# Kernel optimization log

Measured on AMD Instinct MI355X. Metric: run time of the kernel, lower is better.

The kernel has to match this reference:

```python
import jax, jax.numpy as jnp
import numpy as np

N, E, IN, HID, HEADS, OUT, G = 50000, 800000, 128, 32, 4, 128, 64
NEG_SLOPE = 0.2


def setup_inputs() -> dict:
    key = jax.random.key(0)
    ks = jax.random.split(key, 20)
    p = lambda k, shape: jax.random.normal(k, shape, jnp.float32) * 0.1
    inp = {
        "x": jax.random.normal(ks[0], (N, IN), jnp.float32),
        "edge_index": jax.random.randint(ks[1], (2, E), 0, N, dtype=jnp.int64),
        "batch": jnp.sort(jax.random.randint(ks[2], (N,), 0, G, dtype=jnp.int64)),
        # input_proj: Linear(in_dim, hidden*heads)
        "Wp": p(ks[3], (IN, HID * HEADS)), "bp": p(ks[4], (HID * HEADS,)),
        # layer 1: GATConv(128 -> 32, heads=4, concat) -> 128
        "W1": p(ks[5], (IN, HEADS * HID)), "a_src1": p(ks[6], (HEADS, HID)),
        "a_dst1": p(ks[7], (HEADS, HID)), "b1": p(ks[8], (HEADS * HID,)),
        # layer 2: GATConv(128 -> 32, heads=4, concat) -> 128
        "W2": p(ks[9], (HEADS * HID, HEADS * HID)), "a_src2": p(ks[10], (HEADS, HID)),
        "a_dst2": p(ks[11], (HEADS, HID)), "b2": p(ks[12], (HEADS * HID,)),
        # layer 3: GATConv(128 -> 128, heads=1, concat=False mean)
        "W3": p(ks[13], (HEADS * HID, OUT)), "a_src3": p(ks[14], (1, OUT)),
        "a_dst3": p(ks[15], (1, OUT)), "b3": p(ks[16], (OUT,)),
    }
    return inp


def _gat_conv(x, src, dst, W, a_src, a_dst, b, heads, concat):
    n = x.shape[0]
    h = (x @ W).reshape(n, heads, -1)                      # [N,H,C]
    al_s = jnp.einsum("nhc,hc->nh", h, a_src)              # [N,H]
    al_d = jnp.einsum("nhc,hc->nh", h, a_dst)
    e = al_s[src] + al_d[dst]                              # [Etot,H]
    e = jax.nn.leaky_relu(e, NEG_SLOPE)
    # softmax over incoming edges of each destination node
    m = jax.ops.segment_max(e, dst, num_segments=n)
    e = jnp.exp(e - m[dst])
    s = jax.ops.segment_sum(e, dst, num_segments=n)
    alpha = e / s[dst]                                     # [Etot,H]
    msg = h[src] * alpha[:, :, None]                       # [Etot,H,C]
    out = jax.ops.segment_sum(msg, dst, num_segments=n)    # [N,H,C]
    out = out.reshape(n, -1) if concat else out.mean(axis=1)
    return out + b


def reference(x, edge_index, batch, Wp, bp, W1, a_src1, a_dst1, b1,
              W2, a_src2, a_dst2, b2, W3, a_src3, a_dst3, b3):
    n = x.shape[0]
    loops = jnp.arange(n, dtype=edge_index.dtype)
    src = jnp.concatenate([edge_index[0], loops])          # add self-loops (PyG default)
    dst = jnp.concatenate([edge_index[1], loops])
    x_skip = x @ Wp + bp
    h = _gat_conv(x, src, dst, W1, a_src1, a_dst1, b1, HEADS, True)
    h = jax.nn.relu(h + x_skip)
    h = _gat_conv(h, src, dst, W2, a_src2, a_dst2, b2, HEADS, True)
    h = jax.nn.relu(h + x_skip)
    h = _gat_conv(h, src, dst, W3, a_src3, a_dst3, b3, 1, False)
    # global_mean_pool
    sums = jax.ops.segment_sum(h, batch, num_segments=G)
    cnt = jax.ops.segment_sum(jnp.ones((n,), h.dtype), batch, num_segments=G)
    ctx = sums / jnp.maximum(cnt, 1.0)[:, None]
    return h, ctx
```

## Files before the change

### kernel.cpp

```cpp
#include <hip/hip_runtime.h>
#include <hip/hip_bf16.h>
#include <math.h>

#define N_NODES 50000
#define N_EDGES 800000
#define G_GROUPS 64
#define NEG_SLOPE 0.2f
#define BUCKET 64

typedef __attribute__((ext_vector_type(8))) short bf16x8;
typedef __attribute__((ext_vector_type(4))) float f32x4;

static __device__ __forceinline__ float bf16_lo(unsigned int u) {
    return __uint_as_float(u << 16);
}
static __device__ __forceinline__ float bf16_hi(unsigned int u) {
    return __uint_as_float(u & 0xffff0000u);
}
static __device__ __forceinline__ unsigned short f_to_bf16(float f) {
    unsigned int u = __float_as_uint(f);
    unsigned int r = (u + 0x7fffu + ((u >> 16) & 1u)) >> 16;
    return (unsigned short)r;
}

#define GB_BLOCKS 782
#define CV_BLOCKS 3125
#define FB_BLOCKS 3125


__global__ __launch_bounds__(256) void conv_init(const float* __restrict__ x,
                                                 unsigned short* __restrict__ xb,
                                                 const float* __restrict__ W0,
                                                 const float* __restrict__ W1,
                                                 const float* __restrict__ W2,
                                                 const float* __restrict__ W3,
                                                 unsigned short* __restrict__ T0,
                                                 unsigned short* __restrict__ T1,
                                                 unsigned short* __restrict__ T2,
                                                 unsigned short* __restrict__ T3,
                                                 int* __restrict__ cnt,
                                                 float* __restrict__ ctx) {
    int tid = blockIdx.x * 256 + threadIdx.x;
    if (tid < 65536) {
        int m = tid >> 14;
        int idx = tid & 16383;
        int k = idx >> 7, c = idx & 127;
        const float* W = (m == 0) ? W0 : (m == 1) ? W1 : (m == 2) ? W2 : W3;
        unsigned short* T = (m == 0) ? T0 : (m == 1) ? T1 : (m == 2) ? T2 : T3;
        T[c * 128 + k] = f_to_bf16(W[idx]);
    }
    if (tid < N_NODES) cnt[tid] = 0;
    if (tid < G_GROUPS * 128) ctx[tid] = 0.f;
    const float4* p = (const float4*)(x + (size_t)tid * 8);
    float4 v0 = p[0], v1 = p[1];
    ushort4 o0, o1;
    o0.x = f_to_bf16(v0.x); o0.y = f_to_bf16(v0.y);
    o0.z = f_to_bf16(v0.z); o0.w = f_to_bf16(v0.w);
    o1.x = f_to_bf16(v1.x); o1.y = f_to_bf16(v1.y);
    o1.z = f_to_bf16(v1.z); o1.w = f_to_bf16(v1.w);
    ushort4* q = (ushort4*)(xb + (size_t)tid * 8);
    q[0] = o0; q[1] = o1;
}


static __device__ __forceinline__ void gemm_body(const unsigned short* __restrict__ Xb,
                                                 const unsigned short* __restrict__ Wt,
                                                 const float* __restrict__ bias,
                                                 unsigned short* __restrict__ Yb,
                                                 int n, int addBias,
                                                 const float* __restrict__ asrcP,
                                                 const float* __restrict__ adstP,
                                                 float* __restrict__ alsP,
                                                 float* __restrict__ aldP, int H,
                                                 int blk, unsigned short* Wl) {
    char* wl = (char*)Wl;
    int t = threadIdx.x;
#pragma unroll
    for (int i = 0; i < 8; i++) {
        int slot = i * 256 + t;
        int byte = slot * 16;
        int r = byte >> 8;
        int off = byte & 255;
        uint4 v = *(const uint4*)((const char*)Wt + byte);
        *(uint4*)(wl + r * 256 + (off ^ ((r & 7) << 4))) = v;
    }
    __syncthreads();

    int wave = t >> 6, lane = t & 63;
    int lr = lane & 15, lk = lane >> 4;
    int arow = blk * 64 + wave * 16 + lr;
    int arowc = min(arow, n - 1);
    const char* xrow = (const char*)(Xb + (size_t)arowc * 128);
    bf16x8 a[4];
#pragma unroll
    for (int ks = 0; ks < 4; ks++)
        a[ks] = *(const bf16x8*)(xrow + ks * 64 + lk * 16);

    f32x4 zero = {0.f, 0.f, 0.f, 0.f};
    f32x4 acc[8];
#pragma unroll
    for (int j = 0; j < 8; j++) acc[j] = zero;

#pragma unroll
    for (int j = 0; j < 8; j++) {
        int c = j * 16 + lr;
        const char* wrow = wl + c * 256;
        int sw = (c & 7) << 4;
#pragma unroll
        for (int ks = 0; ks < 4; ks++) {
            bf16x8 b = *(const bf16x8*)(wrow + ((ks * 64 + lk * 16) ^ sw));
            acc[j] = __builtin_amdgcn_mfma_f32_16x16x32_bf16(a[ks], b, acc[j], 0, 0, 0);
        }
    }

    int orow0 = blk * 64 + wave * 16 + lk * 4;
    if (!alsP) {
#pragma unroll
        for (int j = 0; j < 8; j++) {
            int c = j * 16 + lr;
            float bv = addBias ? bias[c] : 0.f;
#pragma unroll
            for (int r = 0; r < 4; r++) {
                int orow = orow0 + r;
                if (orow < n) Yb[(size_t)orow * 128 + c] = f_to_bf16(acc[j][r] + bv);
            }
        }
        return;
    }

    __syncthreads();
    unsigned short* Hl = Wl;
    int lrow0 = wave * 16 + lk * 4;
#pragma unroll
    for (int j = 0; j < 8; j++) {
        int c = j * 16 + lr;
#pragma unroll
        for (int r = 0; r < 4; r++) {
            int orow = orow0 + r;
            unsigned short hv = f_to_bf16(acc[j][r]);
            Hl[(lrow0 + r) * 128 + c] = hv;
            if (orow < n) Yb[(size_t)orow * 128 + c] = hv;
        }
    }
    __syncthreads();

    int row = t >> 2, q = t & 3;
    int node = blk * 64 + row;
    if (node < n) {
        const unsigned int* hp = (const unsigned int*)(Hl + row * 128 + q * 32);
        const float* ap = asrcP + q * 32;
        const float* dp = adstP + q * 32;
        float s = 0.f, dd = 0.f;
#pragma unroll 4
        for (int i = 0; i < 16; i++) {
            unsigned int u = hp[i];
            float v0 = bf16_lo(u), v1 = bf16_hi(u);
            s  = fmaf(v0, ap[2 * i], s);
            s  = fmaf(v1, ap[2 * i + 1], s);
            dd = fmaf(v0, dp[2 * i], dd);
            dd = fmaf(v1, dp[2 * i + 1], dd);
        }
        if (H == 4) {
            alsP[node * 4 + q] = s;
            aldP[node * 4 + q] = dd;
        } else {
            s += __shfl_xor(s, 1); s += __shfl_xor(s, 2);
            dd += __shfl_xor(dd, 1); dd += __shfl_xor(dd, 2);
            if (q == 0) { alsP[node] = s; aldP[node] = dd; }
        }
    }
}


__global__ __launch_bounds__(256) void prep2(const unsigned short* __restrict__ Xb,
                                             const unsigned short* __restrict__ WtA,
                                             const unsigned short* __restrict__ WtB,
                                             const float* __restrict__ biasA,
                                             unsigned short* __restrict__ xskip,
                                             unsigned short* __restrict__ hfeat,
                                             const float* __restrict__ as1,
                                             const float* __restrict__ ad1,
                                             float* __restrict__ als,
                                             float* __restrict__ ald,
                                             const int* __restrict__ ei,
                                             int* __restrict__ cnt,
                                             int* __restrict__ colb) {
    __shared__ unsigned short Wl[128 * 128];
    int bid = blockIdx.x;
    if (bid % 3 == 0) {
        int g = bid / 3;
        if (g >= 2 * GB_BLOCKS) return;
        if (g < GB_BLOCKS) {
            gemm_body(Xb, WtA, biasA, xskip, N_NODES, 1,
                      nullptr, nullptr, nullptr, nullptr, 0, g, Wl);
        } else {
            gemm_body(Xb, WtB, nullptr, hfeat, N_NODES, 0,
                      as1, ad1, als, ald, 4, g - GB_BLOCKS, Wl);
        }
    } else {
        int fb = bid - bid / 3 - 1;
        int e = fb * 256 + threadIdx.x;
        if (fb >= FB_BLOCKS || e >= N_EDGES) return;
        int src = ei[e];
        int dst = ei[N_EDGES + e];
        int pos = atomicAdd(&cnt[dst], 1);
        if (pos < BUCKET) colb[dst * BUCKET + pos] = src;
    }
}


__global__ __launch_bounds__(256) void gemm_mfma(const unsigned short* __restrict__ Xb,
                                                 const unsigned short* __restrict__ Wt,
                                                 unsigned short* __restrict__ Yb,
                                                 const float* __restrict__ asrcP,
                                                 const float* __restrict__ adstP,
                                                 float* __restrict__ alsP,
                                                 float* __restrict__ aldP, int H) {
    __shared__ unsigned short Wl[128 * 128];
    gemm_body(Xb, Wt, nullptr, Yb, N_NODES, 0,
              asrcP, adstP, alsP, aldP, H, blockIdx.x, Wl);
}


template <int H, int MODE>
__global__ __launch_bounds__(256) void aggregate(const unsigned short* __restrict__ hfeat,
                                                 const float* __restrict__ als,
                                                 const float* __restrict__ ald,
                                                 const int* __restrict__ cnt,
                                                 const int* __restrict__ colb,
                                                 const float* __restrict__ bias,
                                                 const unsigned short* __restrict__ xskip,
                                                 float* __restrict__ outf,
                                                 unsigned short* __restrict__ outb, int n) {
    int wave = (blockIdx.x * blockDim.x + threadIdx.x) >> 6;
    int lane = threadIdx.x & 63;
    if (wave >= n) return;
    int d = wave;
    int h2 = (H == 4) ? (lane >> 4) : 0;
    int eoff = lane & 15;
    int sbase = (H == 4) ? (lane & 48) : 0;
    float aldh = ald[d * H + h2];
    int c0 = 2 * lane;
    int cd = min(cnt[d], BUCKET);
    const int* bkt = colb + d * BUCKET;

    float vs = als[d * H + h2] + aldh;
    vs = (vs > 0.f) ? vs : NEG_SLOPE * vs;
    float ps = __expf(fminf(vs, 60.f));
    unsigned int us = *(const unsigned int*)&hfeat[(size_t)d * 128 + c0];
    float psum = (eoff == 0) ? ps : 0.f;
    float a0 = ps * bf16_lo(us);
    float a1 = ps * bf16_hi(us);

    for (int ce = 0; ce < cd; ce += 16) {
        int idx = ce + eoff;
        int idxc = min(idx, cd - 1);
        int sE = bkt[idxc];
        float v = als[sE * H + h2] + aldh;
        v = (v > 0.f) ? v : NEG_SLOPE * v;
        float p = (idx < cd) ? __expf(fminf(v, 60.f)) : 0.f;
        psum += p;
        int nv = min(cd - ce, 16);
        if (nv == 16) {
#pragma unroll
            for (int e = 0; e < 16; e++) {
                int s = __shfl(sE, sbase + e);
                float pe = __shfl(p, sbase + e);
                unsigned int u = *(const unsigned int*)&hfeat[(size_t)s * 128 + c0];
                a0 = fmaf(pe, bf16_lo(u), a0);
                a1 = fmaf(pe, bf16_hi(u), a1);
            }
        } else {
            for (int e = 0; e < nv; e++) {
                int s = __shfl(sE, sbase + e);
                float pe = __shfl(p, sbase + e);
                unsigned int u = *(const unsigned int*)&hfeat[(size_t)s * 128 + c0];
                a0 = fmaf(pe, bf16_lo(u), a0);
                a1 = fmaf(pe, bf16_hi(u), a1);
            }
        }
    }

#pragma unroll
    for (int o = 1; o < 16; o <<= 1)
        psum += __shfl_xor(psum, o);

    float inv = 1.f / psum;
    float o0 = a0 * inv + bias[c0];
    float o1 = a1 * inv + bias[c0 + 1];
    if (MODE == 0) {
        unsigned int ux = *(const unsigned int*)&xskip[(size_t)d * 128 + c0];
        o0 = fmaxf(o0 + bf16_lo(ux), 0.f);
        o1 = fmaxf(o1 + bf16_hi(ux), 0.f);
        unsigned int packed = (unsigned int)f_to_bf16(o0) |
                              ((unsigned int)f_to_bf16(o1) << 16);
        *(unsigned int*)&outb[(size_t)d * 128 + c0] = packed;
    } else {
        outf[(size_t)d * 128 + c0] = o0;
        outf[(size_t)d * 128 + c0 + 1] = o1;
    }
}


__global__ void pool_partial(const float* __restrict__ h, const int* __restrict__ batch,
                             float* __restrict__ ctx) {
    int c = threadIdx.x;
    int base = blockIdx.x * 64;
    int lim = min(base + 64, N_NODES);
    if (base >= N_NODES) return;
    float acc = 0.f;
    int curg = batch[base];
    for (int node = base; node < lim; node++) {
        int g = batch[node];
        if (g != curg) {
            atomicAdd(&ctx[curg * 128 + c], acc);
            curg = g; acc = 0.f;
        }
        acc += h[(size_t)node * 128 + c];
    }
    atomicAdd(&ctx[curg * 128 + c], acc);
}

__global__ void pool_div(const int* __restrict__ batch, float* __restrict__ ctx) {
    int g = blockIdx.x;
    int c = threadIdx.x;
    int lo = 0, hi = N_NODES;
    while (lo < hi) { int mid = (lo + hi) >> 1; if (batch[mid] < g) lo = mid + 1; else hi = mid; }
    int gs = lo;
    hi = N_NODES;
    while (lo < hi) { int mid = (lo + hi) >> 1; if (batch[mid] < g + 1) lo = mid + 1; else hi = mid; }
    int ge = lo;
    ctx[g * 128 + c] /= fmaxf((float)(ge - gs), 1.f);
}


extern "C" void kernel_launch(void* const* d_in, const int* in_sizes, int n_in,
                              void* d_out, int out_size, void* d_ws, size_t ws_size,
                              hipStream_t stream) {
    const float* x   = (const float*)d_in[0];
    const int*   ei  = (const int*)d_in[1];
    const int*   bat = (const int*)d_in[2];
    const float* Wp  = (const float*)d_in[3];
    const float* bp  = (const float*)d_in[4];
    const float* W1  = (const float*)d_in[5];
    const float* as1 = (const float*)d_in[6];
    const float* ad1 = (const float*)d_in[7];
    const float* b1  = (const float*)d_in[8];
    const float* W2  = (const float*)d_in[9];
    const float* as2 = (const float*)d_in[10];
    const float* ad2 = (const float*)d_in[11];
    const float* b2  = (const float*)d_in[12];
    const float* W3  = (const float*)d_in[13];
    const float* as3 = (const float*)d_in[14];
    const float* ad3 = (const float*)d_in[15];
    const float* b3  = (const float*)d_in[16];

    float* out_h   = (float*)d_out;
    float* out_ctx = out_h + (size_t)N_NODES * 128;

    char* w = (char*)d_ws;
    unsigned short* xskip = (unsigned short*)w;  w += (size_t)N_NODES * 128 * 2;
    unsigned short* hfeat = (unsigned short*)w;  w += (size_t)N_NODES * 128 * 2;
    unsigned short* hcur  = (unsigned short*)w;  w += (size_t)N_NODES * 128 * 2;
    unsigned short* xb    = (unsigned short*)w;  w += (size_t)N_NODES * 128 * 2;
    unsigned short* Wtp   = (unsigned short*)w;  w += 16384 * 2;
    unsigned short* Wt1   = (unsigned short*)w;  w += 16384 * 2;
    unsigned short* Wt2   = (unsigned short*)w;  w += 16384 * 2;
    unsigned short* Wt3   = (unsigned short*)w;  w += 16384 * 2;
    float* als   = (float*)w;                    w += (size_t)N_NODES * 4 * 4;
    float* ald   = (float*)w;                    w += (size_t)N_NODES * 4 * 4;
    int* cnt     = (int*)w;                      w += (size_t)N_NODES * 4;
    int* colb    = (int*)w;                      w += (size_t)N_NODES * BUCKET * 4;

    conv_init<<<CV_BLOCKS, 256, 0, stream>>>(x, xb, Wp, W1, W2, W3,
                                             Wtp, Wt1, Wt2, Wt3, cnt, out_ctx);

    prep2<<<4692, 256, 0, stream>>>(xb, Wtp, Wt1, bp, xskip, hfeat,
                                    as1, ad1, als, ald, ei, cnt, colb);

    const int AGB = (N_NODES * 64 + 255) / 256;

    aggregate<4, 0><<<AGB, 256, 0, stream>>>(hfeat, als, ald, cnt, colb, b1, xskip,
                                             nullptr, hcur, N_NODES);

    gemm_mfma<<<GB_BLOCKS, 256, 0, stream>>>(hcur, Wt2, hfeat, as2, ad2, als, ald, 4);
    aggregate<4, 0><<<AGB, 256, 0, stream>>>(hfeat, als, ald, cnt, colb, b2, xskip,
                                             nullptr, hcur, N_NODES);

    gemm_mfma<<<GB_BLOCKS, 256, 0, stream>>>(hcur, Wt3, hfeat, as3, ad3, als, ald, 1);
    aggregate<1, 1><<<AGB, 256, 0, stream>>>(hfeat, als, ald, cnt, colb, b3, nullptr,
                                             out_h, nullptr, N_NODES);

    pool_partial<<<GB_BLOCKS, 128, 0, stream>>>(out_h, bat, out_ctx);
    pool_div<<<G_GROUPS, 128, 0, stream>>>(bat, out_ctx);
}
```

Baseline: 255.0 us.

## Prefetch next edge chunk in aggregate, widen H=1 chunks, shrink pool blocks

The aggregate loop now loads the next chunk's source indices and attention logits while the current chunk's feature gathers run, a software pipeline meant to hide index and logit load latency. For the single-head layer each chunk spans all 64 lanes instead of 16, so one wave covers up to 64 edges per chunk and the psum reduction spans the full wave. pool_partial uses 32 nodes per block, which doubles the block count for more parallelism at the cost of more atomics.

```diff
diff --git a/kernel.cpp b/kernel.cpp
--- a/kernel.cpp
+++ b/kernel.cpp
@@ -236,8 +236,9 @@
     int lane = threadIdx.x & 63;
     if (wave >= n) return;
     int d = wave;
+    const int CH = (H == 4) ? 16 : 64;
     int h2 = (H == 4) ? (lane >> 4) : 0;
-    int eoff = lane & 15;
+    int eoff = (H == 4) ? (lane & 15) : lane;
     int sbase = (H == 4) ? (lane & 48) : 0;
     float aldh = ald[d * H + h2];
     int c0 = 2 * lane;
@@ -252,18 +253,25 @@
     float a0 = ps * bf16_lo(us);
     float a1 = ps * bf16_hi(us);
 
-    for (int ce = 0; ce < cd; ce += 16) {
-        int idx = ce + eoff;
-        int idxc = min(idx, cd - 1);
-        int sE = bkt[idxc];
+    int sE = 0;
+    float p = 0.f;
+    if (cd > 0) {
+        int idx = eoff;
+        sE = bkt[min(idx, cd - 1)];
         float v = als[sE * H + h2] + aldh;
         v = (v > 0.f) ? v : NEG_SLOPE * v;
-        float p = (idx < cd) ? __expf(fminf(v, 60.f)) : 0.f;
+        p = (idx < cd) ? __expf(fminf(v, 60.f)) : 0.f;
+    }
+
+    for (int ce = 0; ce < cd; ce += CH) {
         psum += p;
-        int nv = min(cd - ce, 16);
-        if (nv == 16) {
-#pragma unroll
-            for (int e = 0; e < 16; e++) {
+        int nce = ce + CH;
+        int sE_n = 0;
+        if (nce < cd) sE_n = bkt[min(nce + eoff, cd - 1)];
+        int nv = min(cd - ce, CH);
+        if (nv == CH) {
+#pragma unroll
+            for (int e = 0; e < CH; e++) {
                 int s = __shfl(sE, sbase + e);
                 float pe = __shfl(p, sbase + e);
                 unsigned int u = *(const unsigned int*)&hfeat[(size_t)s * 128 + c0];
@@ -279,10 +287,18 @@
                 a1 = fmaf(pe, bf16_hi(u), a1);
             }
         }
-    }
-
-#pragma unroll
-    for (int o = 1; o < 16; o <<= 1)
+        float p_n = 0.f;
+        if (nce < cd) {
+            float v = als[sE_n * H + h2] + aldh;
+            v = (v > 0.f) ? v : NEG_SLOPE * v;
+            p_n = (nce + eoff < cd) ? __expf(fminf(v, 60.f)) : 0.f;
+        }
+        sE = sE_n;
+        p = p_n;
+    }
+
+#pragma unroll
+    for (int o = 1; o < ((H == 4) ? 16 : 64); o <<= 1)
         psum += __shfl_xor(psum, o);
 
     float inv = 1.f / psum;
@@ -305,8 +321,8 @@
 __global__ void pool_partial(const float* __restrict__ h, const int* __restrict__ batch,
                              float* __restrict__ ctx) {
     int c = threadIdx.x;
-    int base = blockIdx.x * 64;
-    int lim = min(base + 64, N_NODES);
+    int base = blockIdx.x * 32;
+    int lim = min(base + 32, N_NODES);
     if (base >= N_NODES) return;
     float acc = 0.f;
     int curg = batch[base];
@@ -391,6 +407,6 @@
     aggregate<1, 1><<<AGB, 256, 0, stream>>>(hfeat, als, ald, cnt, colb, b3, nullptr,
                                              out_h, nullptr, N_NODES);
 
-    pool_partial<<<GB_BLOCKS, 128, 0, stream>>>(out_h, bat, out_ctx);
+    pool_partial<<<(N_NODES + 31) / 32, 128, 0, stream>>>(out_h, bat, out_ctx);
     pool_div<<<G_GROUPS, 128, 0, stream>>>(bat, out_ctx);
 }
```

Measured after the change: 262.2 us. 1.03x slower.
